# Performance work log

Hardware: AMD Instinct MI355X
Metric: run time of the kernel (lower is better)

## Reference

```python
import jax, jax.numpy as jnp
import numpy as np

# static sizes (see shape_source)
IN_SIZE = 50000
M = 3            # n_modalities
N0 = 40960       # layer-0 sampled source nodes
N1 = 16384       # layer-0 dst == layer-1 src
B = 4096         # batch (final dst nodes)
HEADS = 4
DIM = 64
HD = HEADS * DIM # 256, integration_size
DEG0, DEG1 = 16, 16
E0, E1 = N1 * DEG0, B * DEG1
NEG_SLOPE = 0.2  # GATConv default negative_slope


def gat_conv(x_src, e_src, e_dst, n_dst, W, att, bias):
    """PyG GATConv with bipartite input (x, None): attention uses only alpha_l.
    x_src: [Ns, HD]; W: [HD, HD]; att: [1, H, C]; returns [n_dst, HD]."""
    x_l = (x_src @ W.T).reshape(-1, HEADS, DIM)            # [Ns, H, C]
    alpha_l = (x_l * att).sum(-1)                          # [Ns, H]
    logits = jax.nn.leaky_relu(alpha_l[e_src], NEG_SLOPE)  # [E, H]
    m = jax.ops.segment_max(logits, e_dst, num_segments=n_dst)
    m = jnp.where(jnp.isfinite(m), m, 0.0)                 # guard empty segments
    e = jnp.exp(logits - m[e_dst])
    denom = jax.ops.segment_sum(e, e_dst, num_segments=n_dst)
    a = e / (denom[e_dst] + 1e-16)                         # edge softmax per dst
    msg = x_l[e_src] * a[:, :, None]                       # [E, H, C]
    out = jax.ops.segment_sum(msg, e_dst, num_segments=n_dst)
    return out.reshape(n_dst, HD) + bias


def interp(scales_param, mask, key):
    """Interp module, evaluate=False, idxs = range(M)."""
    scales = jax.nn.softmax(scales_param, axis=-1)         # [1, M]
    rm = jax.random.randint(key, mask.shape, 0, 2).astype(jnp.float32)
    rm = rm + (1.0 / (1.0 + rm.sum(-1)) ** 20)[:, None]
    rm = rm + (1.0 / (mask.sum(-1) ** 20))[:, None]
    rm = jax.lax.stop_gradient(jnp.floor(rm))              # .int().float()
    rm = rm / (rm + 1e-10)
    m = mask * rm
    m = jax.nn.softmax(m + (1.0 - m) * (-1e10), axis=-1)   # [B, M]
    return scales, m


def setup_inputs() -> dict:
    key = jax.random.key(0)
    ks = jax.random.split(key, 12)
    s = 0.05
    return {
        "masks": jnp.ones((B, M), jnp.float32),
        "n_ids": jax.random.randint(ks[0], (M, N0), 0, IN_SIZE, dtype=jnp.int32),
        "e0_src": jax.random.randint(ks[1], (M, E0), 0, N0, dtype=jnp.int32),
        "e0_dst": jnp.repeat(jnp.arange(N1, dtype=jnp.int32), DEG0),
        "e1_src": jax.random.randint(ks[2], (M, E1), 0, N1, dtype=jnp.int32),
        "e1_dst": jnp.repeat(jnp.arange(B, dtype=jnp.int32), DEG1),
        "pre_W": jax.random.normal(ks[3], (M, HD, IN_SIZE), jnp.float32) * s,
        "pre_b": jax.random.normal(ks[4], (M, HD), jnp.float32) * s,
        "gat_W": jax.random.normal(ks[5], (M, HD, HD), jnp.float32) * s,
        "gat_att": jax.random.normal(ks[6], (M, 1, HEADS, DIM), jnp.float32) * s,
        "gat_b": jax.random.normal(ks[7], (M, HD), jnp.float32) * s,
        "scales_param": jnp.full((1, M), 1.0 / M, jnp.float32),
        "emb_W": jax.random.normal(ks[8], (128, HD), jnp.float32) * s,
        "emb_b": jax.random.normal(ks[9], (128,), jnp.float32) * s,
    }


def reference(masks, n_ids, e0_src, e0_dst, e1_src, e1_dst,
              pre_W, pre_b, gat_W, gat_att, gat_b,
              scales_param, emb_W, emb_b):
    scales, interp_masks = interp(scales_param, masks, jax.random.key(42))
    x_mod = jnp.zeros((B, HD), dtype=masks.dtype)
    for i in range(M):  # small fixed modality loop (structurally distinct params)
        # one-hot(n_id) @ W.T + b  ==  gather of columns of W (same math)
        x = jnp.take(pre_W[i], n_ids[i], axis=1).T + pre_b[i]        # [N0, HD]
        g0 = gat_conv(x, e0_src[i], e0_dst, N1, gat_W[i], gat_att[i], gat_b[i])
        g1 = gat_conv(g0, e1_src[i], e1_dst, B, gat_W[i], gat_att[i], gat_b[i])
        # x_store_layer = [g0[:B] (sliced), g0[:B] (x_pre), g1]; x = sum + g1
        xm = 2.0 * g0[:B] + 2.0 * g1                                  # [B, HD]
        xm = scales[:, i] * interp_masks[:, i].reshape(-1, 1) * xm
        x_mod = x_mod + xm
    emb = x_mod @ emb_W.T + emb_b                                     # [B, 128]
    dot = emb @ emb.T                                                 # [B, B]
    return dot, emb, scales
```

## Files before the change

kernel.cpp:

```cpp
#include <hip/hip_runtime.h>
#include <hip/hip_bf16.h>
#include <cstdint>

#define IN_SZ 50000
#define PADC  50048
#define NM 3
#define N0 40960
#define N1 16384
#define NB 4096
#define HD 256
#define DEG 16
#define E0 (N1*DEG)
#define E1 (NB*DEG)

using short8v = __attribute__((ext_vector_type(8))) short;
using floatx4 = __attribute__((ext_vector_type(4))) float;
typedef unsigned short ushort_t;

__device__ __forceinline__ ushort_t f2bf(float f){
  uint32_t u = __float_as_uint(f);
  uint32_t r = u + 0x7FFFu + ((u>>16)&1u);
  return (ushort_t)(r>>16);
}
__device__ __forceinline__ float bf2f(ushort_t h){
  return __uint_as_float(((uint32_t)h)<<16);
}
__device__ __forceinline__ void gload_lds16(const ushort_t* g, ushort_t* l){
  __builtin_amdgcn_global_load_lds(
      (const __attribute__((address_space(1))) void*)g,
      (__attribute__((address_space(3))) void*)l, 16, 0, 0);
}

__device__ __forceinline__ uint32_t rotl32(uint32_t x, uint32_t d){ return (x<<d)|(x>>(32u-d)); }

__device__ void tf2x32(uint32_t k0, uint32_t k1, uint32_t c0, uint32_t c1,
                       uint32_t& y0, uint32_t& y1)
{
  uint32_t ks2 = k0 ^ k1 ^ 0x1BD11BDAu;
  uint32_t x0 = c0 + k0, x1 = c1 + k1;
#define R4(a,b,c,d) \
  x0+=x1; x1=rotl32(x1,a); x1^=x0; \
  x0+=x1; x1=rotl32(x1,b); x1^=x0; \
  x0+=x1; x1=rotl32(x1,c); x1^=x0; \
  x0+=x1; x1=rotl32(x1,d); x1^=x0;
  R4(13,15,26,6)  x0+=k1;  x1+=ks2+1u;
  R4(17,29,16,24) x0+=ks2; x1+=k0+2u;
  R4(13,15,26,6)  x0+=k0;  x1+=k1+3u;
  R4(17,29,16,24) x0+=k1;  x1+=ks2+4u;
  R4(13,15,26,6)  x0+=ks2; x1+=k0+5u;
#undef R4
  y0=x0; y1=x1;
}

__global__ __launch_bounds__(256) void prep_k(
    const float* __restrict__ masks, const float* __restrict__ sp,
    float* __restrict__ coef, float* __restrict__ scales_out,
    const float* __restrict__ emb_W, float* __restrict__ wT,
    const float* __restrict__ gat_W, ushort_t* __restrict__ gWhi, ushort_t* __restrict__ gWlo,
    const float* __restrict__ pre_b, const float* __restrict__ gat_att,
    const float* __restrict__ gat_b, float* __restrict__ bsum, float* __restrict__ batt)
{
  int blk = blockIdx.x;
  int t = threadIdx.x;
  if (blk < 16){
    int b = blk*256 + t;
    float s0=sp[0], s1=sp[1], s2=sp[2];
    float mx = fmaxf(s0,fmaxf(s1,s2));
    float e0=expf(s0-mx), e1=expf(s1-mx), e2=expf(s2-mx);
    float inv = 1.f/(e0+e1+e2);
    float sc[3] = {e0*inv, e1*inv, e2*inv};
    if (b == 0){ scales_out[0]=sc[0]; scales_out[1]=sc[1]; scales_out[2]=sc[2]; }
    uint32_t bits[3];
    uint32_t K0,K1, t0,t1;
    tf2x32(0u,42u,0u,1u,K0,K1);
    for (int i=0;i<3;i++){
      uint32_t idx = (uint32_t)(b*3+i);
      tf2x32(K0,K1,0u,idx,t0,t1);
      bits[i] = (t0 ^ t1) & 1u;
    }
    float mk[3] = {masks[b*3+0], masks[b*3+1], masks[b*3+2]};
    float msum = mk[0]+mk[1]+mk[2];
    float rs = (float)(bits[0]+bits[1]+bits[2]);
    float add = powf(1.f/(1.f+rs), 20.f) + powf(1.f/msum, 20.f);
    float lg[3]; float lmax = -1e30f;
    for (int i=0;i<3;i++){
      float rm = floorf((float)bits[i] + add);
      rm = rm/(rm+1e-10f);
      float mm = mk[i]*rm;
      lg[i] = mm + (1.f-mm)*(-1e10f);
      lmax = fmaxf(lmax, lg[i]);
    }
    float es[3], ssum=0.f;
    for (int i=0;i<3;i++){ es[i]=expf(lg[i]-lmax); ssum+=es[i]; }
    for (int i=0;i<3;i++) coef[b*3+i] = sc[i]*es[i]/ssum;
  } else if (blk < 144){
    int g = (blk-16)*256 + t;
    int j = g >> 8, k = g & 255;
    wT[k*128 + j] = emb_W[g];
  } else if (blk < 912){
    int g = (blk-144)*256 + t;
    float v = gat_W[g];
    ushort_t h = f2bf(v);
    gWhi[g] = h;
    gWlo[g] = f2bf(v - bf2f(h));
  } else {
    int i = blk - 912, o = t;
    const float* W = gat_W + (size_t)i*HD*HD + (size_t)o*HD;
    const float* b = pre_b + i*HD;
    float s = 0.f;
    for (int k=0;k<HD;k++) s = fmaf(b[k], W[k], s);
    bsum[i*HD + o] = s + gat_b[i*HD + o];
    __shared__ float red[256];
    red[o] = s * gat_att[i*HD + o];
    __syncthreads();
    if (o < 4){
      float p = 0.f;
      for (int j=0;j<64;j++) p += red[o*64 + j];
      batt[i*4 + o] = p;
    }
  }
}

__global__ __launch_bounds__(256) void transp4_k(const float* __restrict__ Wb,
                                                 ushort_t* __restrict__ WT_b)
{
  int i = blockIdx.z;
  const float* W = Wb + (size_t)i*HD*IN_SZ;
  ushort_t* WT = WT_b + (size_t)i*(size_t)PADC*HD;
  __shared__ float tile[32][33];
  int c0 = blockIdx.x*32, k0 = blockIdx.y*32;
  int t = threadIdx.x;
  int lk = t>>3, lq = t&7;
  int cbase = c0 + lq*4;
  float4 f;
  if (cbase + 3 < IN_SZ){
    f = *reinterpret_cast<const float4*>(&W[(size_t)(k0+lk)*IN_SZ + cbase]);
  } else {
    float tmp[4] = {0.f,0.f,0.f,0.f};
#pragma unroll
    for (int e=0;e<4;e++) if (cbase+e < IN_SZ) tmp[e] = W[(size_t)(k0+lk)*IN_SZ + cbase+e];
    f = make_float4(tmp[0],tmp[1],tmp[2],tmp[3]);
  }
  tile[lk][lq*4+0]=f.x; tile[lk][lq*4+1]=f.y; tile[lk][lq*4+2]=f.z; tile[lk][lq*4+3]=f.w;
  __syncthreads();
  int sc = t>>3, skq = t&7;
  uint32_t lo = (uint32_t)f2bf(tile[skq*4+0][sc]) | ((uint32_t)f2bf(tile[skq*4+1][sc])<<16);
  uint32_t hi = (uint32_t)f2bf(tile[skq*4+2][sc]) | ((uint32_t)f2bf(tile[skq*4+3][sc])<<16);
  uint2 pack = make_uint2(lo, hi);
  *reinterpret_cast<uint2*>(&WT[(size_t)(c0+sc)*HD + k0 + skq*4]) = pack;
}

template<bool GTMODE>
__global__ __launch_bounds__(256) void gemm2(
    const ushort_t* __restrict__ A_b, size_t a_stride,
    const ushort_t* __restrict__ Whi_b, const ushort_t* __restrict__ Wlo_b,
    ushort_t* __restrict__ C_b, size_t c_stride,
    const float* __restrict__ att_b, float* __restrict__ alpha_b, size_t al_stride,
    const float* __restrict__ batt, int m_valid)
{
  int i = blockIdx.z;
  int bn0 = blockIdx.x * 128;
  int brow = blockIdx.y * 128;
  const ushort_t* A = A_b + (size_t)i*a_stride;
  const ushort_t* Whi = Whi_b + (size_t)i*HD*HD;
  const ushort_t* Wlo = Wlo_b + (size_t)i*HD*HD;
  ushort_t* C = C_b + (size_t)i*c_stride;
  const float* att = att_b + (size_t)i*HD;
  float* alpha = alpha_b + (size_t)i*al_stride;

  constexpr int NFRAG = GTMODE ? 16 : 24;
  constexpr int NSRC  = GTMODE ? 4 : 6;
  __shared__ __align__(16) ushort_t smem[2][NFRAG*512];
  int t = threadIdx.x, wave = t>>6, lane = t&63;
  int l15 = lane&15, kq = lane>>4;

  int row0 = brow + wave*16 + l15;
  int row1 = brow + (wave+4)*16 + l15;

  const ushort_t* gsrc[NSRC];
  gsrc[0] = A + (size_t)row0*HD + kq*8;
  gsrc[1] = A + (size_t)row1*HD + kq*8;
  if constexpr (GTMODE){
#pragma unroll
    for (int j=2;j<4;j++){
      int ct = wave + 4*(j-2);
      gsrc[j] = Whi + (size_t)(bn0 + ct*16 + l15)*HD + kq*8;
    }
  } else {
#pragma unroll
    for (int j=2;j<6;j++){
      int idx = wave + 4*(j-2);
      int ct = idx>>1, h = idx&1;
      const ushort_t* W = h ? Wlo : Whi;
      gsrc[j] = W + (size_t)(bn0 + ct*16 + l15)*HD + kq*8;
    }
  }

  floatx4 acc[4][4];
#pragma unroll
  for (int r=0;r<4;r++)
#pragma unroll
    for (int c=0;c<4;c++) acc[r][c] = (floatx4){0.f,0.f,0.f,0.f};

  int wm = wave>>1, wn = wave&1;

#pragma unroll
  for (int j=0;j<NSRC;j++)
    gload_lds16(gsrc[j], &smem[0][(wave + 4*j)*512]);
  __syncthreads();

  for (int cc=0; cc<8; cc++){
    int buf = cc & 1;
    if (cc < 7){
      int k0 = (cc+1)*32;
#pragma unroll
      for (int j=0;j<NSRC;j++)
        gload_lds16(gsrc[j] + k0, &smem[buf^1][(wave + 4*j)*512]);
    }
    short8v a[4];
#pragma unroll
    for (int r=0;r<4;r++)
      a[r] = *reinterpret_cast<const short8v*>(&smem[buf][(wm*4+r)*512 + lane*8]);
#pragma unroll
    for (int c=0;c<4;c++){
      int ct = wn*4+c;
      if constexpr (GTMODE){
        short8v bh = *reinterpret_cast<const short8v*>(&smem[buf][(8+ct)*512 + lane*8]);
#pragma unroll
        for (int r=0;r<4;r++)
          acc[r][c] = __builtin_amdgcn_mfma_f32_16x16x32_bf16(a[r], bh, acc[r][c], 0,0,0);
      } else {
        short8v bh = *reinterpret_cast<const short8v*>(&smem[buf][(8+ct*2)*512 + lane*8]);
        short8v bl = *reinterpret_cast<const short8v*>(&smem[buf][(9+ct*2)*512 + lane*8]);
#pragma unroll
        for (int r=0;r<4;r++){
          acc[r][c] = __builtin_amdgcn_mfma_f32_16x16x32_bf16(a[r], bh, acc[r][c], 0,0,0);
          acc[r][c] = __builtin_amdgcn_mfma_f32_16x16x32_bf16(a[r], bl, acc[r][c], 0,0,0);
        }
      }
    }
    __syncthreads();
  }

  float attv[4];
#pragma unroll
  for (int c=0;c<4;c++) attv[c] = att[bn0 + (wn*4+c)*16 + l15];
  int head = (bn0>>6) + wn;
  float battv = 0.f;
  if constexpr (GTMODE) battv = batt[i*4 + head];
#pragma unroll
  for (int r=0;r<4;r++){
    int rowb = brow + wm*64 + r*16 + kq*4;
#pragma unroll
    for (int j=0;j<4;j++){
      if (GTMODE && rowb + j >= m_valid) continue;
      size_t rw = (size_t)(rowb + j)*HD;
#pragma unroll
      for (int c=0;c<4;c++)
        C[rw + bn0 + (wn*4+c)*16 + l15] = f2bf(acc[r][c][j]);
    }
#pragma unroll
    for (int j=0;j<4;j++){
      float p = acc[r][0][j]*attv[0] + acc[r][1][j]*attv[1]
              + acc[r][2][j]*attv[2] + acc[r][3][j]*attv[3];
      p += __shfl_xor(p, 1, 64);
      p += __shfl_xor(p, 2, 64);
      p += __shfl_xor(p, 4, 64);
      p += __shfl_xor(p, 8, 64);
      if (l15 == 0 && (!GTMODE || rowb + j < m_valid)){
        p += battv;
        float lg = p > 0.f ? p : 0.2f*p;
        alpha[(size_t)(rowb + j)*4 + head] = lg;
      }
    }
  }
}

__global__ __launch_bounds__(128) void gat_msg0(
    const ushort_t* __restrict__ GT_b, const float* __restrict__ alphaG_b,
    const int* __restrict__ n_ids, const int* __restrict__ esrc_b,
    const float* __restrict__ bsum_b, uint32_t* __restrict__ g0_u)
{
  int i = blockIdx.y, d = blockIdx.x, t = threadIdx.x;
  const ushort_t* GT = GT_b + (size_t)i*(size_t)PADC*HD;
  const float* alphaG = alphaG_b + (size_t)i*IN_SZ*4;
  const float* bsum = bsum_b + i*HD;
  __shared__ int src[16];
  __shared__ float aw[16][4];
  if (t < 16) src[t] = n_ids[(size_t)i*N0 + esrc_b[(size_t)i*E0 + d*16 + t]];
  __syncthreads();
  if (t < 64){
    int e = t&15, h = t>>4;
    float l = alphaG[(size_t)src[e]*4 + h];
    float m = l;
#pragma unroll
    for (int off=1; off<16; off<<=1) m = fmaxf(m, __shfl_xor(m, off, 64));
    float ex = expf(l - m);
    float s = ex;
#pragma unroll
    for (int off=1; off<16; off<<=1) s += __shfl_xor(s, off, 64);
    aw[e][h] = ex / (s + 1e-16f);
  }
  __syncthreads();
  int h = t >> 5;
  float a0=0.f, a1=0.f;
#pragma unroll
  for (int e=0;e<16;e++){
    uint32_t u = *reinterpret_cast<const uint32_t*>(GT + (size_t)src[e]*HD + 2*t);
    float w = aw[e][h];
    a0 = fmaf(w, bf2f((ushort_t)(u & 0xffffu)), a0);
    a1 = fmaf(w, bf2f((ushort_t)(u >> 16)), a1);
  }
  float v0 = a0 + bsum[2*t], v1 = a1 + bsum[2*t+1];
  g0_u[((size_t)i*N1 + d)*128 + t] = (uint32_t)f2bf(v0) | ((uint32_t)f2bf(v1)<<16);
}

__global__ __launch_bounds__(128) void gat_msg1(
    const ushort_t* __restrict__ xl1hi, const float* __restrict__ alpha1,
    const int* __restrict__ e1src, const float* __restrict__ gat_b,
    const uint32_t* __restrict__ g0_u, const float* __restrict__ coef,
    float* __restrict__ xmod)
{
  int d = blockIdx.x, t = threadIdx.x;
  __shared__ int src[16];
  __shared__ float aw[16][4];
  float o0 = 0.f, o1 = 0.f;
  for (int i=0;i<NM;i++){
    if (t < 16) src[t] = e1src[(size_t)i*E1 + d*16 + t];
    __syncthreads();
    if (t < 64){
      int e = t&15, h = t>>4;
      float l = alpha1[((size_t)i*N1 + src[e])*4 + h];
      float m = l;
#pragma unroll
      for (int off=1; off<16; off<<=1) m = fmaxf(m, __shfl_xor(m, off, 64));
      float ex = expf(l - m);
      float s = ex;
#pragma unroll
      for (int off=1; off<16; off<<=1) s += __shfl_xor(s, off, 64);
      aw[e][h] = ex / (s + 1e-16f);
    }
    __syncthreads();
    const ushort_t* xl = xl1hi + (size_t)i*N1*HD;
    int h = t >> 5;
    float a0=0.f, a1=0.f;
#pragma unroll
    for (int e=0;e<16;e++){
      uint32_t u = *reinterpret_cast<const uint32_t*>(xl + (size_t)src[e]*HD + 2*t);
      float w = aw[e][h];
      a0 = fmaf(w, bf2f((ushort_t)(u & 0xffffu)), a0);
      a1 = fmaf(w, bf2f((ushort_t)(u >> 16)), a1);
    }
    uint32_t gh = g0_u[((size_t)i*N1 + d)*128 + t];
    float g00 = bf2f((ushort_t)(gh & 0xffffu));
    float g01 = bf2f((ushort_t)(gh >> 16));
    const float* bias = gat_b + i*HD;
    float cv = coef[d*3 + i];
    o0 += cv*(2.f*g00 + 2.f*(a0 + bias[2*t]));
    o1 += cv*(2.f*g01 + 2.f*(a1 + bias[2*t+1]));
    __syncthreads();
  }
  *reinterpret_cast<float2*>(&xmod[(size_t)d*HD + 2*t]) = make_float2(o0, o1);
}

__global__ __launch_bounds__(256) void emb_gemm(
  const float* __restrict__ xmod, const float* __restrict__ wT,
  const float* __restrict__ eb, float* __restrict__ emb,
  ushort_t* __restrict__ ehi, ushort_t* __restrict__ elo)
{
  __shared__ float xs[32][260];
  int t = threadIdx.x;
  int brow = blockIdx.x * 32;
#pragma unroll
  for (int j=0;j<8;j++){
    int linear = j*256+t;
    int row = linear >> 6;
    int kq = linear & 63;
    float4 f = *reinterpret_cast<const float4*>(&xmod[(size_t)(brow+row)*256 + kq*4]);
    xs[row][kq*4+0]=f.x; xs[row][kq*4+1]=f.y; xs[row][kq*4+2]=f.z; xs[row][kq*4+3]=f.w;
  }
  __syncthreads();
  int tj = t & 127, th = t >> 7;
  float acc[16];
#pragma unroll
  for(int r=0;r<16;r++) acc[r]=0.f;
  for (int k=0;k<256;k++){
    float w = wT[k*128 + tj];
#pragma unroll
    for (int r=0;r<16;r++) acc[r] = fmaf(xs[th*16+r][k], w, acc[r]);
  }
  float bias = eb[tj];
#pragma unroll
  for (int r=0;r<16;r++){
    size_t idx = (size_t)(brow+th*16+r)*128 + tj;
    float v = acc[r] + bias;
    emb[idx] = v;
    ushort_t hb = f2bf(v);
    ehi[idx] = hb;
    elo[idx] = f2bf(v - bf2f(hb));
  }
}

__global__ __launch_bounds__(256) void dot_mfma(
    const ushort_t* __restrict__ Ehi, const ushort_t* __restrict__ Elo,
    float* __restrict__ dot)
{
  __shared__ __align__(16) ushort_t lb[2][16384];
  int t = threadIdx.x, wave = t>>6, lane = t&63;
  int arow0 = blockIdx.y*128, brow0 = blockIdx.x*128;
  {
    const ushort_t* srcp = (t<128) ? Ehi : Elo;
    ushort_t* dstb = lb[(t<128)?0:1];
    int o = t & 127;
    const ushort_t* rp = srcp + (size_t)(brow0+o)*128;
#pragma unroll
    for (int g=0; g<16; g++){
      short8v v = *reinterpret_cast<const short8v*>(rp + g*8);
      int c = g>>2, grp = g&3;
      int lidx = c*4096 + (o>>4)*512 + ((grp<<4)|(o&15))*8;
      *reinterpret_cast<short8v*>(&dstb[lidx]) = v;
    }
  }
  __syncthreads();

  floatx4 acc[2][8];
#pragma unroll
  for (int rt=0;rt<2;rt++)
#pragma unroll
    for (int ot=0;ot<8;ot++) acc[rt][ot] = (floatx4){0.f,0.f,0.f,0.f};

  int ar0 = arow0 + wave*32 + (lane&15);
  int ar1 = ar0 + 16;
  int koff = (lane>>4)*8;
#pragma unroll
  for (int c=0;c<4;c++){
    short8v ah0 = *reinterpret_cast<const short8v*>(Ehi + (size_t)ar0*128 + c*32 + koff);
    short8v ah1 = *reinterpret_cast<const short8v*>(Ehi + (size_t)ar1*128 + c*32 + koff);
    short8v al0 = *reinterpret_cast<const short8v*>(Elo + (size_t)ar0*128 + c*32 + koff);
    short8v al1 = *reinterpret_cast<const short8v*>(Elo + (size_t)ar1*128 + c*32 + koff);
#pragma unroll
    for (int ot=0;ot<8;ot++){
      short8v bh = *reinterpret_cast<const short8v*>(&lb[0][c*4096 + ot*512 + lane*8]);
      short8v bl = *reinterpret_cast<const short8v*>(&lb[1][c*4096 + ot*512 + lane*8]);
      acc[0][ot] = __builtin_amdgcn_mfma_f32_16x16x32_bf16(ah0, bh, acc[0][ot], 0,0,0);
      acc[0][ot] = __builtin_amdgcn_mfma_f32_16x16x32_bf16(ah0, bl, acc[0][ot], 0,0,0);
      acc[0][ot] = __builtin_amdgcn_mfma_f32_16x16x32_bf16(al0, bh, acc[0][ot], 0,0,0);
      acc[1][ot] = __builtin_amdgcn_mfma_f32_16x16x32_bf16(ah1, bh, acc[1][ot], 0,0,0);
      acc[1][ot] = __builtin_amdgcn_mfma_f32_16x16x32_bf16(ah1, bl, acc[1][ot], 0,0,0);
      acc[1][ot] = __builtin_amdgcn_mfma_f32_16x16x32_bf16(al1, bh, acc[1][ot], 0,0,0);
    }
  }
#pragma unroll
  for (int rt=0;rt<2;rt++){
    int rb = arow0 + wave*32 + rt*16 + (lane>>4)*4;
#pragma unroll
    for (int r=0;r<4;r++)
#pragma unroll
      for (int ot=0;ot<8;ot++)
        dot[(size_t)(rb+r)*4096 + brow0 + ot*16 + (lane&15)] = acc[rt][ot][r];
  }
}

extern "C" void kernel_launch(void* const* d_in, const int* in_sizes, int n_in,
                              void* d_out, int out_size, void* d_ws, size_t ws_size,
                              hipStream_t stream) {
  (void)in_sizes; (void)n_in; (void)out_size; (void)ws_size;
  const float* masks   = (const float*)d_in[0];
  const int*   n_ids   = (const int*)d_in[1];
  const int*   e0_src  = (const int*)d_in[2];
  const int*   e1_src  = (const int*)d_in[4];
  const float* pre_W   = (const float*)d_in[6];
  const float* pre_b   = (const float*)d_in[7];
  const float* gat_W   = (const float*)d_in[8];
  const float* gat_att = (const float*)d_in[9];
  const float* gat_b   = (const float*)d_in[10];
  const float* sp      = (const float*)d_in[11];
  const float* emb_W   = (const float*)d_in[12];
  const float* emb_b   = (const float*)d_in[13];

  float* out = (float*)d_out;
  float* dot = out;
  float* emb = out + (size_t)NB*NB;
  float* scales_out = emb + (size_t)NB*128;

  char* p = (char*)d_ws;
  auto alloc = [&](size_t bytes)->char*{ char* r = p; p += (bytes + 255) & ~(size_t)255; return r; };
  ushort_t* WT    = (ushort_t*)alloc((size_t)NM*PADC*HD*2);
  ushort_t* GT    = (ushort_t*)alloc((size_t)NM*PADC*HD*2);
  float*    alphG = (float*)alloc((size_t)NM*IN_SZ*4*4);
  uint32_t* g0u   = (uint32_t*)alloc((size_t)NM*N1*HD*2);
  ushort_t* xl1hi = (ushort_t*)alloc((size_t)NM*N1*HD*2);
  float*    alph1 = (float*)alloc((size_t)NM*N1*4*4);
  float*    xmod  = (float*)alloc((size_t)NB*HD*4);
  float*    coef  = (float*)alloc((size_t)NB*3*4);
  float*    wT    = (float*)alloc((size_t)HD*128*4);
  ushort_t* gWhi  = (ushort_t*)alloc((size_t)NM*HD*HD*2);
  ushort_t* gWlo  = (ushort_t*)alloc((size_t)NM*HD*HD*2);
  float*    bsum  = (float*)alloc((size_t)NM*HD*4);
  float*    batt  = (float*)alloc((size_t)NM*4*4);
  ushort_t* ehi   = (ushort_t*)alloc((size_t)NB*128*2);
  ushort_t* elo   = (ushort_t*)alloc((size_t)NB*128*2);

  prep_k<<<915, 256, 0, stream>>>(masks, sp, coef, scales_out, emb_W, wT,
                                  gat_W, gWhi, gWlo, pre_b, gat_att, gat_b, bsum, batt);
  transp4_k<<<dim3(PADC/32, 8, NM), 256, 0, stream>>>(pre_W, WT);

  gemm2<true><<<dim3(2, PADC/128, NM), 256, 0, stream>>>(
      WT, (size_t)PADC*HD, gWhi, gWlo,
      GT, (size_t)PADC*HD, gat_att, alphG, (size_t)IN_SZ*4, batt, IN_SZ);
  gat_msg0<<<dim3(N1, NM), 128, 0, stream>>>(GT, alphG, n_ids, e0_src, bsum, g0u);
  gemm2<false><<<dim3(2, N1/128, NM), 256, 0, stream>>>(
      (const ushort_t*)g0u, (size_t)N1*HD, gWhi, gWlo,
      xl1hi, (size_t)N1*HD, gat_att, alph1, (size_t)N1*4, nullptr, N1);
  gat_msg1<<<NB, 128, 0, stream>>>(xl1hi, alph1, e1_src, gat_b, g0u, coef, xmod);
  emb_gemm<<<NB/32, 256, 0, stream>>>(xmod, wT, emb_b, emb, ehi, elo);
  dot_mfma<<<dim3(32,32), 256, 0, stream>>>(ehi, elo, dot);
}
```

Before: 283.3 us.

## Fuse pre_W transpose into projection GEMM reading fp32 columns directly

Replaces the separate transpose-to-bf16 kernel and the GT-mode GEMM with one fused kernel. It loads fp32 tiles of pre_W straight into LDS through an XOR-swizzled layout, converts them to bf16 in registers, and runs MFMA against the gat_W tile with the attention epilogue. This removes the round trip of writing and re-reading the transposed bf16 WT buffer and drops one launch. In exchange each block computes all 256 outputs for 64 columns, and the A loads are strided column reads from rows of pre_W. The lds16 stores also change to per-lane offsets.

```diff
diff --git a/kernel.cpp b/kernel.cpp
--- a/kernel.cpp
+++ b/kernel.cpp
@@ -25,7 +25,7 @@
 __device__ __forceinline__ float bf2f(ushort_t h){
   return __uint_as_float(((uint32_t)h)<<16);
 }
-__device__ __forceinline__ void gload_lds16(const ushort_t* g, ushort_t* l){
+__device__ __forceinline__ void gload_lds16(const void* g, void* l){
   __builtin_amdgcn_global_load_lds(
       (const __attribute__((address_space(1))) void*)g,
       (__attribute__((address_space(3))) void*)l, 16, 0, 0);
@@ -121,42 +121,117 @@
   }
 }
 
-__global__ __launch_bounds__(256) void transp4_k(const float* __restrict__ Wb,
-                                                 ushort_t* __restrict__ WT_b)
+__global__ __launch_bounds__(256) void gt_fused(
+    const float* __restrict__ preW_b,
+    const ushort_t* __restrict__ Whi_b,
+    const float* __restrict__ att_b, const float* __restrict__ batt,
+    ushort_t* __restrict__ GT_b, float* __restrict__ alphaG_b)
 {
   int i = blockIdx.z;
-  const float* W = Wb + (size_t)i*HD*IN_SZ;
-  ushort_t* WT = WT_b + (size_t)i*(size_t)PADC*HD;
-  __shared__ float tile[32][33];
-  int c0 = blockIdx.x*32, k0 = blockIdx.y*32;
-  int t = threadIdx.x;
-  int lk = t>>3, lq = t&7;
-  int cbase = c0 + lq*4;
-  float4 f;
-  if (cbase + 3 < IN_SZ){
-    f = *reinterpret_cast<const float4*>(&W[(size_t)(k0+lk)*IN_SZ + cbase]);
-  } else {
-    float tmp[4] = {0.f,0.f,0.f,0.f};
-#pragma unroll
-    for (int e=0;e<4;e++) if (cbase+e < IN_SZ) tmp[e] = W[(size_t)(k0+lk)*IN_SZ + cbase+e];
-    f = make_float4(tmp[0],tmp[1],tmp[2],tmp[3]);
-  }
-  tile[lk][lq*4+0]=f.x; tile[lk][lq*4+1]=f.y; tile[lk][lq*4+2]=f.z; tile[lk][lq*4+3]=f.w;
+  int brow = blockIdx.x * 64;
+  const float* pw = preW_b + (size_t)i*HD*IN_SZ;
+  const ushort_t* Whi = Whi_b + (size_t)i*HD*HD;
+  const float* att = att_b + (size_t)i*HD;
+  ushort_t* GT = GT_b + (size_t)i*(size_t)PADC*HD;
+  float* alphaG = alphaG_b + (size_t)i*IN_SZ*4;
+
+  __shared__ __align__(16) float    As[2][32*64];
+  __shared__ __align__(16) ushort_t Bs[2][16*512];
+  int t = threadIdx.x, wave = t>>6, lane = t&63;
+  int l15 = lane&15, kq = lane>>4;
+
+  int aRow[2]; int aCol[2];
+#pragma unroll
+  for (int r=0;r<2;r++){
+    int lin = r*256 + t;
+    aRow[r] = lin >> 4;
+    int colq = lin & 15;
+    int srcc = brow + ((colq ^ (((aRow[r]>>3)&3)<<2)) << 2);
+    if (srcc > IN_SZ-4) srcc = IN_SZ-4;
+    aCol[r] = srcc;
+  }
+  const ushort_t* bSrc[4];
+#pragma unroll
+  for (int r=0;r<4;r++){
+    int f = wave + r*4;
+    bSrc[r] = Whi + (size_t)(f*16 + l15)*HD + kq*8;
+  }
+
+  floatx4 acc[16];
+#pragma unroll
+  for (int ot=0;ot<16;ot++) acc[ot] = (floatx4){0.f,0.f,0.f,0.f};
+
+  int clds = (((wave*4 + (l15>>2)) ^ (kq<<2)) << 2) + (l15 & 3);
+
+#pragma unroll
+  for (int r=0;r<2;r++)
+    gload_lds16(pw + (size_t)aRow[r]*IN_SZ + aCol[r],
+                &As[0][(r*256 + wave*64)*4] + lane*4);
+#pragma unroll
+  for (int r=0;r<4;r++)
+    gload_lds16(bSrc[r], &Bs[0][(wave + r*4)*512] + lane*8);
   __syncthreads();
-  int sc = t>>3, skq = t&7;
-  uint32_t lo = (uint32_t)f2bf(tile[skq*4+0][sc]) | ((uint32_t)f2bf(tile[skq*4+1][sc])<<16);
-  uint32_t hi = (uint32_t)f2bf(tile[skq*4+2][sc]) | ((uint32_t)f2bf(tile[skq*4+3][sc])<<16);
-  uint2 pack = make_uint2(lo, hi);
-  *reinterpret_cast<uint2*>(&WT[(size_t)(c0+sc)*HD + k0 + skq*4]) = pack;
-}
-
-template<bool GTMODE>
+
+  for (int cc=0; cc<8; cc++){
+    int buf = cc & 1;
+    if (cc < 7){
+      int k0 = (cc+1)*32;
+#pragma unroll
+      for (int r=0;r<2;r++)
+        gload_lds16(pw + (size_t)(k0 + aRow[r])*IN_SZ + aCol[r],
+                    &As[buf^1][(r*256 + wave*64)*4] + lane*4);
+#pragma unroll
+      for (int r=0;r<4;r++)
+        gload_lds16(bSrc[r] + k0, &Bs[buf^1][(wave + r*4)*512] + lane*8);
+    }
+    float af[8];
+#pragma unroll
+    for (int j=0;j<8;j++) af[j] = As[buf][(kq*8+j)*64 + clds];
+    short8v a;
+#pragma unroll
+    for (int j=0;j<8;j++) a[j] = (short)f2bf(af[j]);
+#pragma unroll
+    for (int ot=0;ot<16;ot++){
+      short8v bh = *reinterpret_cast<const short8v*>(&Bs[buf][ot*512 + lane*8]);
+      acc[ot] = __builtin_amdgcn_mfma_f32_16x16x32_bf16(a, bh, acc[ot], 0,0,0);
+    }
+    __syncthreads();
+  }
+
+  float attv[16];
+#pragma unroll
+  for (int ot=0;ot<16;ot++) attv[ot] = att[ot*16 + l15];
+  int rbase = brow + wave*16 + kq*4;
+#pragma unroll
+  for (int jj=0;jj<4;jj++){
+    int c = rbase + jj;
+    bool ok = c < IN_SZ;
+    size_t rw = (size_t)c*HD;
+    if (ok){
+#pragma unroll
+      for (int ot=0;ot<16;ot++) GT[rw + ot*16 + l15] = f2bf(acc[ot][jj]);
+    }
+#pragma unroll
+    for (int h=0;h<4;h++){
+      float p = acc[4*h+0][jj]*attv[4*h+0] + acc[4*h+1][jj]*attv[4*h+1]
+              + acc[4*h+2][jj]*attv[4*h+2] + acc[4*h+3][jj]*attv[4*h+3];
+      p += __shfl_xor(p, 1, 64);
+      p += __shfl_xor(p, 2, 64);
+      p += __shfl_xor(p, 4, 64);
+      p += __shfl_xor(p, 8, 64);
+      if (l15 == 0 && ok){
+        p += batt[i*4 + h];
+        alphaG[(size_t)c*4 + h] = p > 0.f ? p : 0.2f*p;
+      }
+    }
+  }
+}
+
 __global__ __launch_bounds__(256) void gemm2(
     const ushort_t* __restrict__ A_b, size_t a_stride,
     const ushort_t* __restrict__ Whi_b, const ushort_t* __restrict__ Wlo_b,
     ushort_t* __restrict__ C_b, size_t c_stride,
-    const float* __restrict__ att_b, float* __restrict__ alpha_b, size_t al_stride,
-    const float* __restrict__ batt, int m_valid)
+    const float* __restrict__ att_b, float* __restrict__ alpha_b, size_t al_stride)
 {
   int i = blockIdx.z;
   int bn0 = blockIdx.x * 128;
@@ -168,32 +243,22 @@
   const float* att = att_b + (size_t)i*HD;
   float* alpha = alpha_b + (size_t)i*al_stride;
 
-  constexpr int NFRAG = GTMODE ? 16 : 24;
-  constexpr int NSRC  = GTMODE ? 4 : 6;
-  __shared__ __align__(16) ushort_t smem[2][NFRAG*512];
+  __shared__ __align__(16) ushort_t smem[2][24*512];
   int t = threadIdx.x, wave = t>>6, lane = t&63;
   int l15 = lane&15, kq = lane>>4;
 
   int row0 = brow + wave*16 + l15;
   int row1 = brow + (wave+4)*16 + l15;
 
-  const ushort_t* gsrc[NSRC];
+  const ushort_t* gsrc[6];
   gsrc[0] = A + (size_t)row0*HD + kq*8;
   gsrc[1] = A + (size_t)row1*HD + kq*8;
-  if constexpr (GTMODE){
-#pragma unroll
-    for (int j=2;j<4;j++){
-      int ct = wave + 4*(j-2);
-      gsrc[j] = Whi + (size_t)(bn0 + ct*16 + l15)*HD + kq*8;
-    }
-  } else {
-#pragma unroll
-    for (int j=2;j<6;j++){
-      int idx = wave + 4*(j-2);
-      int ct = idx>>1, h = idx&1;
-      const ushort_t* W = h ? Wlo : Whi;
-      gsrc[j] = W + (size_t)(bn0 + ct*16 + l15)*HD + kq*8;
-    }
+#pragma unroll
+  for (int j=2;j<6;j++){
+    int idx = wave + 4*(j-2);
+    int ct = idx>>1, h = idx&1;
+    const ushort_t* W = h ? Wlo : Whi;
+    gsrc[j] = W + (size_t)(bn0 + ct*16 + l15)*HD + kq*8;
   }
 
   floatx4 acc[4][4];
@@ -205,8 +270,8 @@
   int wm = wave>>1, wn = wave&1;
 
 #pragma unroll
-  for (int j=0;j<NSRC;j++)
-    gload_lds16(gsrc[j], &smem[0][(wave + 4*j)*512]);
+  for (int j=0;j<6;j++)
+    gload_lds16(gsrc[j], &smem[0][(wave + 4*j)*512] + lane*8);
   __syncthreads();
 
   for (int cc=0; cc<8; cc++){
@@ -214,8 +279,8 @@
     if (cc < 7){
       int k0 = (cc+1)*32;
 #pragma unroll
-      for (int j=0;j<NSRC;j++)
-        gload_lds16(gsrc[j] + k0, &smem[buf^1][(wave + 4*j)*512]);
+      for (int j=0;j<6;j++)
+        gload_lds16(gsrc[j] + k0, &smem[buf^1][(wave + 4*j)*512] + lane*8);
     }
     short8v a[4];
 #pragma unroll
@@ -224,19 +289,12 @@
 #pragma unroll
     for (int c=0;c<4;c++){
       int ct = wn*4+c;
-      if constexpr (GTMODE){
-        short8v bh = *reinterpret_cast<const short8v*>(&smem[buf][(8+ct)*512 + lane*8]);
-#pragma unroll
-        for (int r=0;r<4;r++)
-          acc[r][c] = __builtin_amdgcn_mfma_f32_16x16x32_bf16(a[r], bh, acc[r][c], 0,0,0);
-      } else {
-        short8v bh = *reinterpret_cast<const short8v*>(&smem[buf][(8+ct*2)*512 + lane*8]);
-        short8v bl = *reinterpret_cast<const short8v*>(&smem[buf][(9+ct*2)*512 + lane*8]);
-#pragma unroll
-        for (int r=0;r<4;r++){
-          acc[r][c] = __builtin_amdgcn_mfma_f32_16x16x32_bf16(a[r], bh, acc[r][c], 0,0,0);
-          acc[r][c] = __builtin_amdgcn_mfma_f32_16x16x32_bf16(a[r], bl, acc[r][c], 0,0,0);
-        }
+      short8v bh = *reinterpret_cast<const short8v*>(&smem[buf][(8+ct*2)*512 + lane*8]);
+      short8v bl = *reinterpret_cast<const short8v*>(&smem[buf][(9+ct*2)*512 + lane*8]);
+#pragma unroll
+      for (int r=0;r<4;r++){
+        acc[r][c] = __builtin_amdgcn_mfma_f32_16x16x32_bf16(a[r], bh, acc[r][c], 0,0,0);
+        acc[r][c] = __builtin_amdgcn_mfma_f32_16x16x32_bf16(a[r], bl, acc[r][c], 0,0,0);
       }
     }
     __syncthreads();
@@ -246,14 +304,11 @@
 #pragma unroll
   for (int c=0;c<4;c++) attv[c] = att[bn0 + (wn*4+c)*16 + l15];
   int head = (bn0>>6) + wn;
-  float battv = 0.f;
-  if constexpr (GTMODE) battv = batt[i*4 + head];
 #pragma unroll
   for (int r=0;r<4;r++){
     int rowb = brow + wm*64 + r*16 + kq*4;
 #pragma unroll
     for (int j=0;j<4;j++){
-      if (GTMODE && rowb + j >= m_valid) continue;
       size_t rw = (size_t)(rowb + j)*HD;
 #pragma unroll
       for (int c=0;c<4;c++)
@@ -267,8 +322,7 @@
       p += __shfl_xor(p, 2, 64);
       p += __shfl_xor(p, 4, 64);
       p += __shfl_xor(p, 8, 64);
-      if (l15 == 0 && (!GTMODE || rowb + j < m_valid)){
-        p += battv;
+      if (l15 == 0){
         float lg = p > 0.f ? p : 0.2f*p;
         alpha[(size_t)(rowb + j)*4 + head] = lg;
       }
@@ -485,7 +539,6 @@
 
   char* p = (char*)d_ws;
   auto alloc = [&](size_t bytes)->char*{ char* r = p; p += (bytes + 255) & ~(size_t)255; return r; };
-  ushort_t* WT    = (ushort_t*)alloc((size_t)NM*PADC*HD*2);
   ushort_t* GT    = (ushort_t*)alloc((size_t)NM*PADC*HD*2);
   float*    alphG = (float*)alloc((size_t)NM*IN_SZ*4*4);
   uint32_t* g0u   = (uint32_t*)alloc((size_t)NM*N1*HD*2);
@@ -503,15 +556,12 @@
 
   prep_k<<<915, 256, 0, stream>>>(masks, sp, coef, scales_out, emb_W, wT,
                                   gat_W, gWhi, gWlo, pre_b, gat_att, gat_b, bsum, batt);
-  transp4_k<<<dim3(PADC/32, 8, NM), 256, 0, stream>>>(pre_W, WT);
-
-  gemm2<true><<<dim3(2, PADC/128, NM), 256, 0, stream>>>(
-      WT, (size_t)PADC*HD, gWhi, gWlo,
-      GT, (size_t)PADC*HD, gat_att, alphG, (size_t)IN_SZ*4, batt, IN_SZ);
+  gt_fused<<<dim3(PADC/64, 1, NM), 256, 0, stream>>>(
+      pre_W, gWhi, gat_att, batt, GT, alphG);
   gat_msg0<<<dim3(N1, NM), 128, 0, stream>>>(GT, alphG, n_ids, e0_src, bsum, g0u);
-  gemm2<false><<<dim3(2, N1/128, NM), 256, 0, stream>>>(
+  gemm2<<<dim3(2, N1/128, NM), 256, 0, stream>>>(
       (const ushort_t*)g0u, (size_t)N1*HD, gWhi, gWlo,
-      xl1hi, (size_t)N1*HD, gat_att, alph1, (size_t)N1*4, nullptr, N1);
+      xl1hi, (size_t)N1*HD, gat_att, alph1, (size_t)N1*4);
   gat_msg1<<<NB, 128, 0, stream>>>(xl1hi, alph1, e1_src, gat_b, g0u, coef, xmod);
   emb_gemm<<<NB/32, 256, 0, stream>>>(xmod, wT, emb_b, emb, ehi, elo);
   dot_mfma<<<dim3(32,32), 256, 0, stream>>>(ehi, elo, dot);
```

New measurement: 265.4 us. 1.07x faster.

## Aggregate gathered input rows before the layer-0 GAT projection GEMM

Applied to the files above, without the earlier changes.

Layer 0 used to project all 50000 padded input columns through the GAT weight and then gather the projected rows. It now gathers the raw embedding rows per destination node and computes attention logits with a precomputed W^T·att vector. It softmax-aggregates those rows and only then runs the projection GEMM on the 16384 aggregated rows, adding the bias there. This relies on the projection being linear, and it shrinks the GEMM about threefold. In exchange the aggregate is rounded to bf16 before the projection, and the gemm2 LDS destination addressing changes to a per-lane offset.

```diff
diff --git a/kernel.cpp b/kernel.cpp
--- a/kernel.cpp
+++ b/kernel.cpp
@@ -25,7 +25,7 @@
 __device__ __forceinline__ float bf2f(ushort_t h){
   return __uint_as_float(((uint32_t)h)<<16);
 }
-__device__ __forceinline__ void gload_lds16(const ushort_t* g, ushort_t* l){
+__device__ __forceinline__ void gload_lds16(const void* g, void* l){
   __builtin_amdgcn_global_load_lds(
       (const __attribute__((address_space(1))) void*)g,
       (__attribute__((address_space(3))) void*)l, 16, 0, 0);
@@ -58,7 +58,8 @@
     const float* __restrict__ emb_W, float* __restrict__ wT,
     const float* __restrict__ gat_W, ushort_t* __restrict__ gWhi, ushort_t* __restrict__ gWlo,
     const float* __restrict__ pre_b, const float* __restrict__ gat_att,
-    const float* __restrict__ gat_b, float* __restrict__ bsum, float* __restrict__ batt)
+    const float* __restrict__ gat_b, float* __restrict__ bsum, float* __restrict__ batt,
+    float* __restrict__ watt)
 {
   int blk = blockIdx.x;
   int t = threadIdx.x;
@@ -103,7 +104,7 @@
     ushort_t h = f2bf(v);
     gWhi[g] = h;
     gWlo[g] = f2bf(v - bf2f(h));
-  } else {
+  } else if (blk < 915){
     int i = blk - 912, o = t;
     const float* W = gat_W + (size_t)i*HD*HD + (size_t)o*HD;
     const float* b = pre_b + i*HD;
@@ -118,6 +119,16 @@
       for (int j=0;j<64;j++) p += red[o*64 + j];
       batt[i*4 + o] = p;
     }
+  } else {
+    int idx = blk - 915;
+    int i = idx >> 2, h = idx & 3;
+    int k = t;
+    float s = 0.f;
+    for (int o=0;o<64;o++){
+      int oo = h*64 + o;
+      s = fmaf(gat_W[(size_t)i*HD*HD + (size_t)oo*HD + k], gat_att[i*HD + oo], s);
+    }
+    watt[(size_t)i*1024 + k*4 + h] = s;
   }
 }
 
@@ -150,13 +161,72 @@
   *reinterpret_cast<uint2*>(&WT[(size_t)(c0+sc)*HD + k0 + skq*4]) = pack;
 }
 
-template<bool GTMODE>
+__global__ __launch_bounds__(64) void msg0agg(
+    const ushort_t* __restrict__ WT_b, const int* __restrict__ n_ids,
+    const int* __restrict__ esrc_b, const float* __restrict__ watt_b,
+    const float* __restrict__ batt, ushort_t* __restrict__ agg_b)
+{
+  int i = blockIdx.y, d = blockIdx.x, lane = threadIdx.x;
+  const ushort_t* WT = WT_b + (size_t)i*(size_t)PADC*HD;
+  __shared__ uint32_t rows[16*129];
+  __shared__ float wl[1024];
+  __shared__ float aw_s[64];
+  __shared__ int src_s[16];
+  if (lane < 16) src_s[lane] = n_ids[(size_t)i*N0 + esrc_b[(size_t)i*E0 + d*16 + lane]];
+  const float* wg = watt_b + (size_t)i*1024;
+#pragma unroll
+  for (int j=0;j<16;j++) wl[j*64 + lane] = wg[j*64 + lane];
+  __syncthreads();
+#pragma unroll
+  for (int e=0;e<16;e++){
+    const uint32_t* rp = reinterpret_cast<const uint32_t*>(WT + (size_t)src_s[e]*HD);
+    rows[e*129 + lane]      = rp[lane];
+    rows[e*129 + 64 + lane] = rp[64 + lane];
+  }
+  __syncthreads();
+  int e = lane>>2, h = lane&3;
+  float dot = 0.f;
+  for (int j=0;j<128;j++){
+    uint32_t u = rows[e*129 + j];
+    dot = fmaf(bf2f((ushort_t)(u & 0xffffu)), wl[(2*j)*4 + h], dot);
+    dot = fmaf(bf2f((ushort_t)(u >> 16)),     wl[(2*j+1)*4 + h], dot);
+  }
+  dot += batt[i*4 + h];
+  float l = dot > 0.f ? dot : 0.2f*dot;
+  float m = l;
+#pragma unroll
+  for (int off=4; off<64; off<<=1) m = fmaxf(m, __shfl_xor(m, off, 64));
+  float ex = expf(l - m);
+  float s = ex;
+#pragma unroll
+  for (int off=4; off<64; off<<=1) s += __shfl_xor(s, off, 64);
+  aw_s[lane] = ex / (s + 1e-16f);
+  __syncthreads();
+  int hh = lane >> 4;
+  float a0=0.f,a1=0.f,a2=0.f,a3=0.f;
+#pragma unroll
+  for (int e2=0;e2<16;e2++){
+    float w = aw_s[e2*4 + hh];
+    uint32_t u0 = rows[e2*129 + 2*lane];
+    uint32_t u1 = rows[e2*129 + 2*lane + 1];
+    a0 = fmaf(w, bf2f((ushort_t)(u0 & 0xffffu)), a0);
+    a1 = fmaf(w, bf2f((ushort_t)(u0 >> 16)), a1);
+    a2 = fmaf(w, bf2f((ushort_t)(u1 & 0xffffu)), a2);
+    a3 = fmaf(w, bf2f((ushort_t)(u1 >> 16)), a3);
+  }
+  uint32_t p0 = (uint32_t)f2bf(a0) | ((uint32_t)f2bf(a1)<<16);
+  uint32_t p1 = (uint32_t)f2bf(a2) | ((uint32_t)f2bf(a3)<<16);
+  uint32_t* op = reinterpret_cast<uint32_t*>(agg_b + ((size_t)i*N1 + d)*HD);
+  op[2*lane] = p0; op[2*lane+1] = p1;
+}
+
+template<bool BIASMODE>
 __global__ __launch_bounds__(256) void gemm2(
     const ushort_t* __restrict__ A_b, size_t a_stride,
     const ushort_t* __restrict__ Whi_b, const ushort_t* __restrict__ Wlo_b,
     ushort_t* __restrict__ C_b, size_t c_stride,
     const float* __restrict__ att_b, float* __restrict__ alpha_b, size_t al_stride,
-    const float* __restrict__ batt, int m_valid)
+    const float* __restrict__ bias_b)
 {
   int i = blockIdx.z;
   int bn0 = blockIdx.x * 128;
@@ -165,35 +235,23 @@
   const ushort_t* Whi = Whi_b + (size_t)i*HD*HD;
   const ushort_t* Wlo = Wlo_b + (size_t)i*HD*HD;
   ushort_t* C = C_b + (size_t)i*c_stride;
-  const float* att = att_b + (size_t)i*HD;
-  float* alpha = alpha_b + (size_t)i*al_stride;
-
-  constexpr int NFRAG = GTMODE ? 16 : 24;
-  constexpr int NSRC  = GTMODE ? 4 : 6;
-  __shared__ __align__(16) ushort_t smem[2][NFRAG*512];
+
+  __shared__ __align__(16) ushort_t smem[2][24*512];
   int t = threadIdx.x, wave = t>>6, lane = t&63;
   int l15 = lane&15, kq = lane>>4;
 
   int row0 = brow + wave*16 + l15;
   int row1 = brow + (wave+4)*16 + l15;
 
-  const ushort_t* gsrc[NSRC];
+  const ushort_t* gsrc[6];
   gsrc[0] = A + (size_t)row0*HD + kq*8;
   gsrc[1] = A + (size_t)row1*HD + kq*8;
-  if constexpr (GTMODE){
-#pragma unroll
-    for (int j=2;j<4;j++){
-      int ct = wave + 4*(j-2);
-      gsrc[j] = Whi + (size_t)(bn0 + ct*16 + l15)*HD + kq*8;
-    }
-  } else {
-#pragma unroll
-    for (int j=2;j<6;j++){
-      int idx = wave + 4*(j-2);
-      int ct = idx>>1, h = idx&1;
-      const ushort_t* W = h ? Wlo : Whi;
-      gsrc[j] = W + (size_t)(bn0 + ct*16 + l15)*HD + kq*8;
-    }
+#pragma unroll
+  for (int j=2;j<6;j++){
+    int idx = wave + 4*(j-2);
+    int ct = idx>>1, h = idx&1;
+    const ushort_t* W = h ? Wlo : Whi;
+    gsrc[j] = W + (size_t)(bn0 + ct*16 + l15)*HD + kq*8;
   }
 
   floatx4 acc[4][4];
@@ -205,8 +263,8 @@
   int wm = wave>>1, wn = wave&1;
 
 #pragma unroll
-  for (int j=0;j<NSRC;j++)
-    gload_lds16(gsrc[j], &smem[0][(wave + 4*j)*512]);
+  for (int j=0;j<6;j++)
+    gload_lds16(gsrc[j], &smem[0][(wave + 4*j)*512] + lane*8);
   __syncthreads();
 
   for (int cc=0; cc<8; cc++){
@@ -214,8 +272,8 @@
     if (cc < 7){
       int k0 = (cc+1)*32;
 #pragma unroll
-      for (int j=0;j<NSRC;j++)
-        gload_lds16(gsrc[j] + k0, &smem[buf^1][(wave + 4*j)*512]);
+      for (int j=0;j<6;j++)
+        gload_lds16(gsrc[j] + k0, &smem[buf^1][(wave + 4*j)*512] + lane*8);
     }
     short8v a[4];
 #pragma unroll
@@ -224,95 +282,54 @@
 #pragma unroll
     for (int c=0;c<4;c++){
       int ct = wn*4+c;
-      if constexpr (GTMODE){
-        short8v bh = *reinterpret_cast<const short8v*>(&smem[buf][(8+ct)*512 + lane*8]);
-#pragma unroll
-        for (int r=0;r<4;r++)
-          acc[r][c] = __builtin_amdgcn_mfma_f32_16x16x32_bf16(a[r], bh, acc[r][c], 0,0,0);
-      } else {
-        short8v bh = *reinterpret_cast<const short8v*>(&smem[buf][(8+ct*2)*512 + lane*8]);
-        short8v bl = *reinterpret_cast<const short8v*>(&smem[buf][(9+ct*2)*512 + lane*8]);
-#pragma unroll
-        for (int r=0;r<4;r++){
-          acc[r][c] = __builtin_amdgcn_mfma_f32_16x16x32_bf16(a[r], bh, acc[r][c], 0,0,0);
-          acc[r][c] = __builtin_amdgcn_mfma_f32_16x16x32_bf16(a[r], bl, acc[r][c], 0,0,0);
+      short8v bh = *reinterpret_cast<const short8v*>(&smem[buf][(8+ct*2)*512 + lane*8]);
+      short8v bl = *reinterpret_cast<const short8v*>(&smem[buf][(9+ct*2)*512 + lane*8]);
+#pragma unroll
+      for (int r=0;r<4;r++){
+        acc[r][c] = __builtin_amdgcn_mfma_f32_16x16x32_bf16(a[r], bh, acc[r][c], 0,0,0);
+        acc[r][c] = __builtin_amdgcn_mfma_f32_16x16x32_bf16(a[r], bl, acc[r][c], 0,0,0);
+      }
+    }
+    __syncthreads();
+  }
+
+  float attv[4];
+#pragma unroll
+  for (int c=0;c<4;c++){
+    int col = bn0 + (wn*4+c)*16 + l15;
+    if constexpr (BIASMODE) attv[c] = bias_b[i*HD + col];
+    else                    attv[c] = att_b[(size_t)i*HD + col];
+  }
+  int head = (bn0>>6) + wn;
+#pragma unroll
+  for (int r=0;r<4;r++){
+    int rowb = brow + wm*64 + r*16 + kq*4;
+#pragma unroll
+    for (int j=0;j<4;j++){
+      size_t rw = (size_t)(rowb + j)*HD;
+#pragma unroll
+      for (int c=0;c<4;c++){
+        float v = acc[r][c][j];
+        if constexpr (BIASMODE) v += attv[c];
+        C[rw + bn0 + (wn*4+c)*16 + l15] = f2bf(v);
+      }
+    }
+    if constexpr (!BIASMODE){
+#pragma unroll
+      for (int j=0;j<4;j++){
+        float p = acc[r][0][j]*attv[0] + acc[r][1][j]*attv[1]
+                + acc[r][2][j]*attv[2] + acc[r][3][j]*attv[3];
+        p += __shfl_xor(p, 1, 64);
+        p += __shfl_xor(p, 2, 64);
+        p += __shfl_xor(p, 4, 64);
+        p += __shfl_xor(p, 8, 64);
+        if (l15 == 0){
+          float lg = p > 0.f ? p : 0.2f*p;
+          alpha_b[(size_t)i*al_stride + (size_t)(rowb + j)*4 + head] = lg;
         }
       }
     }
-    __syncthreads();
-  }
-
-  float attv[4];
-#pragma unroll
-  for (int c=0;c<4;c++) attv[c] = att[bn0 + (wn*4+c)*16 + l15];
-  int head = (bn0>>6) + wn;
-  float battv = 0.f;
-  if constexpr (GTMODE) battv = batt[i*4 + head];
-#pragma unroll
-  for (int r=0;r<4;r++){
-    int rowb = brow + wm*64 + r*16 + kq*4;
-#pragma unroll
-    for (int j=0;j<4;j++){
-      if (GTMODE && rowb + j >= m_valid) continue;
-      size_t rw = (size_t)(rowb + j)*HD;
-#pragma unroll
-      for (int c=0;c<4;c++)
-        C[rw + bn0 + (wn*4+c)*16 + l15] = f2bf(acc[r][c][j]);
-    }
-#pragma unroll
-    for (int j=0;j<4;j++){
-      float p = acc[r][0][j]*attv[0] + acc[r][1][j]*attv[1]
-              + acc[r][2][j]*attv[2] + acc[r][3][j]*attv[3];
-      p += __shfl_xor(p, 1, 64);
-      p += __shfl_xor(p, 2, 64);
-      p += __shfl_xor(p, 4, 64);
-      p += __shfl_xor(p, 8, 64);
-      if (l15 == 0 && (!GTMODE || rowb + j < m_valid)){
-        p += battv;
-        float lg = p > 0.f ? p : 0.2f*p;
-        alpha[(size_t)(rowb + j)*4 + head] = lg;
-      }
-    }
-  }
-}
-
-__global__ __launch_bounds__(128) void gat_msg0(
-    const ushort_t* __restrict__ GT_b, const float* __restrict__ alphaG_b,
-    const int* __restrict__ n_ids, const int* __restrict__ esrc_b,
-    const float* __restrict__ bsum_b, uint32_t* __restrict__ g0_u)
-{
-  int i = blockIdx.y, d = blockIdx.x, t = threadIdx.x;
-  const ushort_t* GT = GT_b + (size_t)i*(size_t)PADC*HD;
-  const float* alphaG = alphaG_b + (size_t)i*IN_SZ*4;
-  const float* bsum = bsum_b + i*HD;
-  __shared__ int src[16];
-  __shared__ float aw[16][4];
-  if (t < 16) src[t] = n_ids[(size_t)i*N0 + esrc_b[(size_t)i*E0 + d*16 + t]];
-  __syncthreads();
-  if (t < 64){
-    int e = t&15, h = t>>4;
-    float l = alphaG[(size_t)src[e]*4 + h];
-    float m = l;
-#pragma unroll
-    for (int off=1; off<16; off<<=1) m = fmaxf(m, __shfl_xor(m, off, 64));
-    float ex = expf(l - m);
-    float s = ex;
-#pragma unroll
-    for (int off=1; off<16; off<<=1) s += __shfl_xor(s, off, 64);
-    aw[e][h] = ex / (s + 1e-16f);
-  }
-  __syncthreads();
-  int h = t >> 5;
-  float a0=0.f, a1=0.f;
-#pragma unroll
-  for (int e=0;e<16;e++){
-    uint32_t u = *reinterpret_cast<const uint32_t*>(GT + (size_t)src[e]*HD + 2*t);
-    float w = aw[e][h];
-    a0 = fmaf(w, bf2f((ushort_t)(u & 0xffffu)), a0);
-    a1 = fmaf(w, bf2f((ushort_t)(u >> 16)), a1);
-  }
-  float v0 = a0 + bsum[2*t], v1 = a1 + bsum[2*t+1];
-  g0_u[((size_t)i*N1 + d)*128 + t] = (uint32_t)f2bf(v0) | ((uint32_t)f2bf(v1)<<16);
+  }
 }
 
 __global__ __launch_bounds__(128) void gat_msg1(
@@ -486,8 +503,7 @@
   char* p = (char*)d_ws;
   auto alloc = [&](size_t bytes)->char*{ char* r = p; p += (bytes + 255) & ~(size_t)255; return r; };
   ushort_t* WT    = (ushort_t*)alloc((size_t)NM*PADC*HD*2);
-  ushort_t* GT    = (ushort_t*)alloc((size_t)NM*PADC*HD*2);
-  float*    alphG = (float*)alloc((size_t)NM*IN_SZ*4*4);
+  ushort_t* agg   = (ushort_t*)alloc((size_t)NM*N1*HD*2);
   uint32_t* g0u   = (uint32_t*)alloc((size_t)NM*N1*HD*2);
   ushort_t* xl1hi = (ushort_t*)alloc((size_t)NM*N1*HD*2);
   float*    alph1 = (float*)alloc((size_t)NM*N1*4*4);
@@ -498,20 +514,21 @@
   ushort_t* gWlo  = (ushort_t*)alloc((size_t)NM*HD*HD*2);
   float*    bsum  = (float*)alloc((size_t)NM*HD*4);
   float*    batt  = (float*)alloc((size_t)NM*4*4);
+  float*    watt  = (float*)alloc((size_t)NM*1024*4);
   ushort_t* ehi   = (ushort_t*)alloc((size_t)NB*128*2);
   ushort_t* elo   = (ushort_t*)alloc((size_t)NB*128*2);
 
-  prep_k<<<915, 256, 0, stream>>>(masks, sp, coef, scales_out, emb_W, wT,
-                                  gat_W, gWhi, gWlo, pre_b, gat_att, gat_b, bsum, batt);
+  prep_k<<<927, 256, 0, stream>>>(masks, sp, coef, scales_out, emb_W, wT,
+                                  gat_W, gWhi, gWlo, pre_b, gat_att, gat_b,
+                                  bsum, batt, watt);
   transp4_k<<<dim3(PADC/32, 8, NM), 256, 0, stream>>>(pre_W, WT);
-
-  gemm2<true><<<dim3(2, PADC/128, NM), 256, 0, stream>>>(
-      WT, (size_t)PADC*HD, gWhi, gWlo,
-      GT, (size_t)PADC*HD, gat_att, alphG, (size_t)IN_SZ*4, batt, IN_SZ);
-  gat_msg0<<<dim3(N1, NM), 128, 0, stream>>>(GT, alphG, n_ids, e0_src, bsum, g0u);
+  msg0agg<<<dim3(N1, NM), 64, 0, stream>>>(WT, n_ids, e0_src, watt, batt, agg);
+  gemm2<true><<<dim3(2, N1/128, NM), 256, 0, stream>>>(
+      agg, (size_t)N1*HD, gWhi, gWlo,
+      (ushort_t*)g0u, (size_t)N1*HD, nullptr, nullptr, 0, bsum);
   gemm2<false><<<dim3(2, N1/128, NM), 256, 0, stream>>>(
       (const ushort_t*)g0u, (size_t)N1*HD, gWhi, gWlo,
-      xl1hi, (size_t)N1*HD, gat_att, alph1, (size_t)N1*4, nullptr, N1);
+      xl1hi, (size_t)N1*HD, gat_att, alph1, (size_t)N1*4, nullptr);
   gat_msg1<<<NB, 128, 0, stream>>>(xl1hi, alph1, e1_src, gat_b, g0u, coef, xmod);
   emb_gemm<<<NB/32, 256, 0, stream>>>(xmod, wT, emb_b, emb, ehi, elo);
   dot_mfma<<<dim3(32,32), 256, 0, stream>>>(ehi, elo, dot);
```

Measured after the change: 288.5 us. About the same (+1.8%).
